# Kernel tuning notes

Hardware: AMD Instinct MI355X
Metric: run time of the kernel (lower is better)

The kernel has to match this reference:

```python
import jax, jax.numpy as jnp
import numpy as np

MARGIN = 0.3  # init kwarg, mode='norm'


def _pairwise_dist(X):
    # squared euclidean distances, then safe sqrt (matches euc_dist(X.t()).sqrt())
    sq = jnp.sum(X * X, axis=1)                      # [n]
    d2 = sq[:, None] + sq[None, :] - 2.0 * (X @ X.T)  # [n, n]
    d2 = jnp.maximum(d2, 0.0)
    # safe sqrt: avoid inf derivative at 0 (diagonal); forward value identical
    return jnp.where(d2 > 0.0, jnp.sqrt(jnp.where(d2 > 0.0, d2, 1.0)), 0.0)


def setup_inputs() -> dict:
    key = jax.random.key(0)
    kx, ky = jax.random.split(key)
    X = jax.random.normal(kx, (4096, 2048), dtype=jnp.float32)
    Y = jax.random.randint(ky, (4096,), 0, 128, dtype=jnp.int64)
    return {"X": X, "Y": Y}


def reference(X, Y):
    dist = _pairwise_dist(X)                         # [n, n]
    mask = Y[:, None] == Y[None, :]                  # same-identity mask [n, n]
    inf = jnp.array(jnp.inf, dtype=dist.dtype)
    # hardest positive per anchor: max over same-label entries
    dist_ap = jnp.max(jnp.where(mask, dist, -inf), axis=1)  # [n]
    # hardest negative per anchor: min over different-label entries
    dist_an = jnp.min(jnp.where(mask, inf, dist), axis=1)   # [n]
    # mode == 'norm': mean hinge
    return jnp.mean(jnp.maximum(dist_ap - dist_an + MARGIN, 0.0))
```

## Files before the change

kernel.cpp:

```cpp
#include <hip/hip_runtime.h>
#include <hip/hip_bf16.h>
#include <hip/hip_fp8.h>

typedef __attribute__((ext_vector_type(4))) int i32x4;
typedef __attribute__((ext_vector_type(8))) int i32x8;
typedef __attribute__((ext_vector_type(16))) float f32x16;

#define MARGIN 0.3f
#define BIGF 3.0e38f

__device__ __forceinline__ void gl2lds16(const void* g, void* l) {
    __builtin_amdgcn_global_load_lds(
        (const __attribute__((address_space(1))) void*)g,
        (__attribute__((address_space(3))) void*)l,
        16, 0, 0);
}

__global__ __launch_bounds__(256) void convert_norm_kernel(
    const float* __restrict__ X, unsigned char* __restrict__ Xq,
    float* __restrict__ nrm, unsigned* __restrict__ ap,
    unsigned* __restrict__ an, unsigned* __restrict__ cnt, int K) {
    const int wave = threadIdx.x >> 6, lane = threadIdx.x & 63;
    const int row = blockIdx.x * 4 + wave;
    const float* xr = X + (size_t)row * K;
    unsigned char* xqr = Xq + (size_t)row * K;
    float s = 0.0f;
    for (int c = lane * 8; c < K; c += 64 * 8) {
        float4 v0 = *(const float4*)(xr + c);
        float4 v1 = *(const float4*)(xr + c + 4);
        float f[8] = {v0.x, v0.y, v0.z, v0.w, v1.x, v1.y, v1.z, v1.w};
        union { unsigned char b[8]; uint2 u; } p;
#pragma unroll
        for (int i = 0; i < 8; i++) {
            __hip_fp8_e4m3 q(f[i]);
            p.b[i] = q.__x;
            float d = (float)q;
            s += d * d;
        }
        *(uint2*)(xqr + c) = p.u;
    }
    for (int off = 32; off > 0; off >>= 1) s += __shfl_xor(s, off, 64);
    if (lane == 0) {
        nrm[row] = s;
        ap[row] = 0u;
        an[row] = 0x7F800000u;
        if (row == 0) *cnt = 0u;
    }
}

__global__ __launch_bounds__(256, 4) void gemm_reduce_kernel(
    const unsigned char* __restrict__ Xq, const float* __restrict__ nrm,
    const int* __restrict__ Y, unsigned* __restrict__ ap,
    unsigned* __restrict__ an, unsigned* __restrict__ cnt,
    float* __restrict__ out, int N, int K) {
    __shared__ __align__(16) unsigned char sA[128 * 128];
    __shared__ __align__(16) unsigned char sB[128 * 128];
    __shared__ int sYr[128], sYc[128];
    __shared__ float sNr[128], sNc[128];
    __shared__ float redmax[4][64], redmin[4][64];
    __shared__ float lsum[4];
    __shared__ unsigned s_done;

    const int tid = threadIdx.x;
    const int wave = tid >> 6;
    const int lane = tid & 63;
    const int m = lane & 31;
    const int h = lane >> 5;
    const int wr = wave >> 1;
    const int wc = wave & 1;

    const int NB = N >> 7;
    const int rowBase = (blockIdx.x >> 5) * 128;
    const int colBase = (blockIdx.x & (NB - 1)) * 128;

    if (tid < 128) {
        sYr[tid] = Y[rowBase + tid];
        sNr[tid] = nrm[rowBase + tid];
    } else {
        int t = tid - 128;
        sYc[t] = Y[colBase + t];
        sNc[t] = nrm[colBase + t];
    }

    f32x16 acc[2][2];
#pragma unroll
    for (int si = 0; si < 2; si++)
#pragma unroll
        for (int sj = 0; sj < 2; sj++)
#pragma unroll
            for (int rr = 0; rr < 16; rr++) acc[si][sj][rr] = 0.0f;

    const int rsub = lane >> 3;
    const int jchunk = (lane & 7) ^ rsub;
    const unsigned char* gA = Xq + (size_t)(rowBase + wave * 32 + rsub) * K + jchunk * 16;
    const unsigned char* gB = Xq + (size_t)(colBase + wave * 32 + rsub) * K + jchunk * 16;
    unsigned char* lA = sA + wave * 4096;
    unsigned char* lB = sB + wave * 4096;
    const size_t g8 = (size_t)8 * K;

    const int e = m & 7;
    const int nit = K >> 7;

    for (int it = 0; it < nit; it++) {
        const size_t go = (size_t)it * 128;
#pragma unroll
        for (int g = 0; g < 4; g++) {
            gl2lds16(gA + go + g * g8, lA + g * 1024);
            gl2lds16(gB + go + g * g8, lB + g * 1024);
        }
        __syncthreads();

#pragma unroll
        for (int s = 0; s < 2; s++) {
            const int c0 = s * 4 + h * 2;
            i32x8 af[2], bf[2];
#pragma unroll
            for (int si = 0; si < 2; si++) {
                const unsigned char* base = sA + (wr * 64 + si * 32 + m) * 128;
                i32x4 lo = *(const i32x4*)(base + ((c0 ^ e) * 16));
                i32x4 hi = *(const i32x4*)(base + (((c0 + 1) ^ e) * 16));
                af[si] = __builtin_shufflevector(lo, hi, 0, 1, 2, 3, 4, 5, 6, 7);
            }
#pragma unroll
            for (int sj = 0; sj < 2; sj++) {
                const unsigned char* base = sB + (wc * 64 + sj * 32 + m) * 128;
                i32x4 lo = *(const i32x4*)(base + ((c0 ^ e) * 16));
                i32x4 hi = *(const i32x4*)(base + (((c0 + 1) ^ e) * 16));
                bf[sj] = __builtin_shufflevector(lo, hi, 0, 1, 2, 3, 4, 5, 6, 7);
            }
#pragma unroll
            for (int si = 0; si < 2; si++)
#pragma unroll
                for (int sj = 0; sj < 2; sj++)
                    acc[si][sj] = __builtin_amdgcn_mfma_scale_f32_32x32x64_f8f6f4(
                        af[si], bf[sj], acc[si][sj], 0 ,
                        0 , 0, 127 ,
                        0, 127 );
        }
        __syncthreads();
    }

#pragma unroll
    for (int si = 0; si < 2; si++)
#pragma unroll
        for (int reg = 0; reg < 16; reg++) {
            const int row64 = si * 32 + (reg & 3) + 8 * (reg >> 2) + 4 * h;
            const int rIdx = wr * 64 + row64;
            const int yr = sYr[rIdx];
            const float nr = sNr[rIdx];
            float dp = -1.0f, dn = BIGF;
#pragma unroll
            for (int sj = 0; sj < 2; sj++) {
                const int cIdx = wc * 64 + sj * 32 + m;
                float d2 = nr + sNc[cIdx] - 2.0f * acc[si][sj][reg];
                float d = sqrtf(fmaxf(d2, 0.0f));
                bool same = (yr == sYc[cIdx]);
                dp = fmaxf(dp, same ? d : -1.0f);
                dn = fminf(dn, same ? BIGF : d);
            }
            for (int off = 1; off < 32; off <<= 1) {
                dp = fmaxf(dp, __shfl_xor(dp, off, 64));
                dn = fminf(dn, __shfl_xor(dn, off, 64));
            }
            if (m == 0) {
                redmax[wave][row64] = dp;
                redmin[wave][row64] = dn;
            }
        }
    __syncthreads();

    if (tid < 128) {
        const int wr2 = tid >> 6, r64 = tid & 63;
        float mx = fmaxf(redmax[wr2 * 2][r64], redmax[wr2 * 2 + 1][r64]);
        float mn = fminf(redmin[wr2 * 2][r64], redmin[wr2 * 2 + 1][r64]);
        atomicMax(&ap[rowBase + tid], __float_as_uint(fmaxf(mx, 0.0f)));
        atomicMin(&an[rowBase + tid], __float_as_uint(mn));
    }

    __syncthreads();
    if (tid == 0) {
        __threadfence();
        s_done = atomicAdd(cnt, 1u);
    }
    __syncthreads();
    if (s_done == gridDim.x - 1) {
        __threadfence();
        float s = 0.0f;
        for (int i = tid; i < N; i += 256) {
            unsigned ua = __hip_atomic_load(&ap[i], __ATOMIC_RELAXED,
                                            __HIP_MEMORY_SCOPE_AGENT);
            unsigned ub = __hip_atomic_load(&an[i], __ATOMIC_RELAXED,
                                            __HIP_MEMORY_SCOPE_AGENT);
            s += fmaxf(__uint_as_float(ua) - __uint_as_float(ub) + MARGIN, 0.0f);
        }
        for (int off = 32; off > 0; off >>= 1) s += __shfl_xor(s, off, 64);
        if (lane == 0) lsum[wave] = s;
        __syncthreads();
        if (tid == 0)
            out[0] = (lsum[0] + lsum[1] + lsum[2] + lsum[3]) / (float)N;
    }
}

extern "C" void kernel_launch(void* const* d_in, const int* in_sizes, int n_in,
                              void* d_out, int out_size, void* d_ws, size_t ws_size,
                              hipStream_t stream) {
    const float* X = (const float*)d_in[0];
    const int* Y = (const int*)d_in[1];
    float* out = (float*)d_out;
    const int N = in_sizes[1];
    const int K = in_sizes[0] / N;

    char* ws = (char*)d_ws;
    unsigned char* Xq = (unsigned char*)ws;
    float* nrm = (float*)(ws + (size_t)N * K);
    unsigned* ap = (unsigned*)((char*)nrm + (size_t)N * 4);
    unsigned* an = (unsigned*)((char*)ap + (size_t)N * 4);
    unsigned* cnt = (unsigned*)((char*)an + (size_t)N * 4);

    convert_norm_kernel<<<N / 4, 256, 0, stream>>>(X, Xq, nrm, ap, an, cnt, K);
    const int NB = N / 128;
    gemm_reduce_kernel<<<NB * NB, 256, 0, stream>>>(Xq, nrm, Y, ap, an, cnt,
                                                    out, N, K);
}
```

Measured before the change: 135.1 us.

## Enlarge GEMM tile to 256x256 with double-buffered LDS prefetch

```diff
diff --git a/kernel.cpp b/kernel.cpp
--- a/kernel.cpp
+++ b/kernel.cpp
@@ -48,17 +48,17 @@
     }
 }
 
-__global__ __launch_bounds__(256, 4) void gemm_reduce_kernel(
+__global__ __launch_bounds__(512, 2) void gemm_reduce_kernel(
     const unsigned char* __restrict__ Xq, const float* __restrict__ nrm,
     const int* __restrict__ Y, unsigned* __restrict__ ap,
     unsigned* __restrict__ an, unsigned* __restrict__ cnt,
     float* __restrict__ out, int N, int K) {
-    __shared__ __align__(16) unsigned char sA[128 * 128];
-    __shared__ __align__(16) unsigned char sB[128 * 128];
-    __shared__ int sYr[128], sYc[128];
-    __shared__ float sNr[128], sNc[128];
-    __shared__ float redmax[4][64], redmin[4][64];
-    __shared__ float lsum[4];
+    __shared__ __align__(16) unsigned char sA[2][32768];
+    __shared__ __align__(16) unsigned char sB[2][32768];
+    __shared__ int sYr[256], sYc[256];
+    __shared__ float sNr[256], sNc[256];
+    __shared__ float redmax[4][256], redmin[4][256];
+    __shared__ float lsum[8];
     __shared__ unsigned s_done;
 
     const int tid = threadIdx.x;
@@ -66,86 +66,107 @@
     const int lane = tid & 63;
     const int m = lane & 31;
     const int h = lane >> 5;
-    const int wr = wave >> 1;
-    const int wc = wave & 1;
-
-    const int NB = N >> 7;
-    const int rowBase = (blockIdx.x >> 5) * 128;
-    const int colBase = (blockIdx.x & (NB - 1)) * 128;
-
-    if (tid < 128) {
+    const int wr = wave >> 2;
+    const int wc = wave & 3;
+
+    const int NB = N >> 8;
+    const int rowBase = (blockIdx.x / NB) << 8;
+    const int colBase = (blockIdx.x % NB) << 8;
+
+    if (tid < 256) {
         sYr[tid] = Y[rowBase + tid];
         sNr[tid] = nrm[rowBase + tid];
     } else {
-        int t = tid - 128;
+        const int t = tid - 256;
         sYc[t] = Y[colBase + t];
         sNc[t] = nrm[colBase + t];
     }
 
-    f32x16 acc[2][2];
-#pragma unroll
-    for (int si = 0; si < 2; si++)
+    f32x16 acc[4][2];
+#pragma unroll
+    for (int si = 0; si < 4; si++)
 #pragma unroll
         for (int sj = 0; sj < 2; sj++)
 #pragma unroll
             for (int rr = 0; rr < 16; rr++) acc[si][sj][rr] = 0.0f;
 
     const int rsub = lane >> 3;
-    const int jchunk = (lane & 7) ^ rsub;
-    const unsigned char* gA = Xq + (size_t)(rowBase + wave * 32 + rsub) * K + jchunk * 16;
-    const unsigned char* gB = Xq + (size_t)(colBase + wave * 32 + rsub) * K + jchunk * 16;
-    unsigned char* lA = sA + wave * 4096;
-    unsigned char* lB = sB + wave * 4096;
+    const int jc = (lane & 7) ^ rsub;
+    const unsigned char* gA = Xq + (size_t)(rowBase + wave * 32 + rsub) * K;
+    const unsigned char* gB = Xq + (size_t)(colBase + wave * 32 + rsub) * K;
     const size_t g8 = (size_t)8 * K;
 
-    const int e = m & 7;
+    const int e2 = (m & 7) ^ ((m >> 3) & 3);
     const int nit = K >> 7;
 
-    for (int it = 0; it < nit; it++) {
-        const size_t go = (size_t)it * 128;
-#pragma unroll
-        for (int g = 0; g < 4; g++) {
-            gl2lds16(gA + go + g * g8, lA + g * 1024);
-            gl2lds16(gB + go + g * g8, lB + g * 1024);
-        }
-        __syncthreads();
+#pragma unroll
+    for (int g = 0; g < 4; g++) {
+        gl2lds16(gA + g * g8 + ((jc ^ g) << 4), &sA[0][wave * 4096 + g * 1024]);
+        gl2lds16(gB + g * g8 + ((jc ^ g) << 4), &sB[0][wave * 4096 + g * 1024]);
+    }
+    __syncthreads();
+
+    int cur = 0;
+    for (int it = 0; it < nit; ++it) {
+        const bool pf = (it + 1 < nit);
+        const size_t go = (size_t)(it + 1) * 128;
+        const unsigned char* cA = sA[cur];
+        const unsigned char* cB = sB[cur];
+        unsigned char* nA = sA[cur ^ 1] + wave * 4096;
+        unsigned char* nB = sB[cur ^ 1] + wave * 4096;
 
 #pragma unroll
         for (int s = 0; s < 2; s++) {
+            if (pf) {
+                if (s == 0) {
+#pragma unroll
+                    for (int g = 0; g < 4; g++)
+                        gl2lds16(gA + go + g * g8 + ((jc ^ g) << 4), nA + g * 1024);
+                } else {
+#pragma unroll
+                    for (int g = 0; g < 4; g++)
+                        gl2lds16(gB + go + g * g8 + ((jc ^ g) << 4), nB + g * 1024);
+                }
+            }
             const int c0 = s * 4 + h * 2;
-            i32x8 af[2], bf[2];
-#pragma unroll
-            for (int si = 0; si < 2; si++) {
-                const unsigned char* base = sA + (wr * 64 + si * 32 + m) * 128;
-                i32x4 lo = *(const i32x4*)(base + ((c0 ^ e) * 16));
-                i32x4 hi = *(const i32x4*)(base + (((c0 + 1) ^ e) * 16));
+            i32x8 af[4], bf[2];
+#pragma unroll
+            for (int si = 0; si < 4; si++) {
+                const unsigned char* base = cA + (wr * 128 + si * 32 + m) * 128;
+                i32x4 lo = *(const i32x4*)(base + ((c0 ^ e2) << 4));
+                i32x4 hi = *(const i32x4*)(base + (((c0 + 1) ^ e2) << 4));
                 af[si] = __builtin_shufflevector(lo, hi, 0, 1, 2, 3, 4, 5, 6, 7);
             }
 #pragma unroll
             for (int sj = 0; sj < 2; sj++) {
-                const unsigned char* base = sB + (wc * 64 + sj * 32 + m) * 128;
-                i32x4 lo = *(const i32x4*)(base + ((c0 ^ e) * 16));
-                i32x4 hi = *(const i32x4*)(base + (((c0 + 1) ^ e) * 16));
+                const unsigned char* base = cB + (wc * 64 + sj * 32 + m) * 128;
+                i32x4 lo = *(const i32x4*)(base + ((c0 ^ e2) << 4));
+                i32x4 hi = *(const i32x4*)(base + (((c0 + 1) ^ e2) << 4));
                 bf[sj] = __builtin_shufflevector(lo, hi, 0, 1, 2, 3, 4, 5, 6, 7);
             }
-#pragma unroll
-            for (int si = 0; si < 2; si++)
+            __builtin_amdgcn_s_barrier();
+            __builtin_amdgcn_s_setprio(1);
+#pragma unroll
+            for (int si = 0; si < 4; si++)
 #pragma unroll
                 for (int sj = 0; sj < 2; sj++)
                     acc[si][sj] = __builtin_amdgcn_mfma_scale_f32_32x32x64_f8f6f4(
                         af[si], bf[sj], acc[si][sj], 0 ,
                         0 , 0, 127 ,
                         0, 127 );
+            __builtin_amdgcn_s_setprio(0);
+            if (s == 0) __builtin_amdgcn_s_barrier();
         }
         __syncthreads();
-    }
-
-#pragma unroll
-    for (int si = 0; si < 2; si++)
+        cur ^= 1;
+    }
+
+#pragma unroll
+    for (int si = 0; si < 4; si++)
 #pragma unroll
         for (int reg = 0; reg < 16; reg++) {
-            const int row64 = si * 32 + (reg & 3) + 8 * (reg >> 2) + 4 * h;
-            const int rIdx = wr * 64 + row64;
+            const int row128 = si * 32 + (reg & 3) + 8 * (reg >> 2) + 4 * h;
+            const int rIdx = wr * 128 + row128;
             const int yr = sYr[rIdx];
             const float nr = sNr[rIdx];
             float dp = -1.0f, dn = BIGF;
@@ -163,16 +184,17 @@
                 dn = fminf(dn, __shfl_xor(dn, off, 64));
             }
             if (m == 0) {
-                redmax[wave][row64] = dp;
-                redmin[wave][row64] = dn;
-            }
-        }
-    __syncthreads();
-
-    if (tid < 128) {
-        const int wr2 = tid >> 6, r64 = tid & 63;
-        float mx = fmaxf(redmax[wr2 * 2][r64], redmax[wr2 * 2 + 1][r64]);
-        float mn = fminf(redmin[wr2 * 2][r64], redmin[wr2 * 2 + 1][r64]);
+                redmax[wc][rIdx] = dp;
+                redmin[wc][rIdx] = dn;
+            }
+        }
+    __syncthreads();
+
+    if (tid < 256) {
+        float mx = fmaxf(fmaxf(redmax[0][tid], redmax[1][tid]),
+                         fmaxf(redmax[2][tid], redmax[3][tid]));
+        float mn = fminf(fminf(redmin[0][tid], redmin[1][tid]),
+                         fminf(redmin[2][tid], redmin[3][tid]));
         atomicMax(&ap[rowBase + tid], __float_as_uint(fmaxf(mx, 0.0f)));
         atomicMin(&an[rowBase + tid], __float_as_uint(mn));
     }
@@ -186,7 +208,7 @@
     if (s_done == gridDim.x - 1) {
         __threadfence();
         float s = 0.0f;
-        for (int i = tid; i < N; i += 256) {
+        for (int i = tid; i < N; i += 512) {
             unsigned ua = __hip_atomic_load(&ap[i], __ATOMIC_RELAXED,
                                             __HIP_MEMORY_SCOPE_AGENT);
             unsigned ub = __hip_atomic_load(&an[i], __ATOMIC_RELAXED,
@@ -196,8 +218,12 @@
         for (int off = 32; off > 0; off >>= 1) s += __shfl_xor(s, off, 64);
         if (lane == 0) lsum[wave] = s;
         __syncthreads();
-        if (tid == 0)
-            out[0] = (lsum[0] + lsum[1] + lsum[2] + lsum[3]) / (float)N;
+        if (tid == 0) {
+            float t = 0.0f;
+#pragma unroll
+            for (int w = 0; w < 8; w++) t += lsum[w];
+            out[0] = t / (float)N;
+        }
     }
 }
 
@@ -218,7 +244,7 @@
     unsigned* cnt = (unsigned*)((char*)an + (size_t)N * 4);
 
     convert_norm_kernel<<<N / 4, 256, 0, stream>>>(X, Xq, nrm, ap, an, cnt, K);
-    const int NB = N / 128;
-    gemm_reduce_kernel<<<NB * NB, 256, 0, stream>>>(Xq, nrm, Y, ap, an, cnt,
+    const int NB = N / 256;
+    gemm_reduce_kernel<<<NB * NB, 512, 0, stream>>>(Xq, nrm, Y, ap, an, cnt,
                                                     out, N, K);
 }
```

New measurement: 138.5 us. 2.6% more time.
